# Performance work log

Measured on AMD Instinct MI355X. Metric: run time of the kernel, lower is better.

Reference implementation:

```python
import jax, jax.numpy as jnp
import numpy as np

B, S, D, H = 4, 2048, 1024, 16
HD = D // H

def setup_inputs() -> dict:
    key = jax.random.key(0)
    ks = jax.random.split(key, 5)
    x = jax.random.normal(ks[0], (B, S, D), dtype=jnp.float32)
    mask = jnp.ones((B, S), dtype=jnp.int32)
    # torch nn.Linear init scale ~ 1/sqrt(fan_in); use small normal for stability
    qkv_w = jax.random.normal(ks[1], (3 * D, D), dtype=jnp.float32) * (1.0 / np.sqrt(D))
    qkv_b = jax.random.normal(ks[2], (3 * D,), dtype=jnp.float32) * 0.02
    out_w = jax.random.normal(ks[3], (D, D), dtype=jnp.float32) * (1.0 / np.sqrt(D))
    out_b = jax.random.normal(ks[4], (D,), dtype=jnp.float32) * 0.02
    return {"x": x, "mask": mask, "qkv_w": qkv_w, "qkv_b": qkv_b,
            "out_w": out_w, "out_b": out_b}

def reference(x, mask, qkv_w, qkv_b, out_w, out_b):
    b, s, d = x.shape
    scale = np.sqrt(HD).astype(np.float32)
    # qkv projection: torch Linear y = x @ W^T + b
    qkv = x @ qkv_w.T + qkv_b                      # (b, s, 3d)
    qkv = qkv.reshape(b, s, 3, H, HD)
    qkv = jnp.transpose(qkv, (2, 0, 3, 1, 4))      # (3, b, H, s, hd)
    q, k, v = qkv[0], qkv[1], qkv[2]
    scores = jnp.einsum('bhqd,bhkd->bhqk', q, k) / scale  # (b, H, s, s)
    neg_inf = jnp.float32(-jnp.inf)
    causal = jnp.tril(jnp.ones((s, s), dtype=bool))
    scores = jnp.where(causal[None, None], scores, neg_inf)
    key_mask = (mask != 0)[:, None, None, :]       # (b, 1, 1, s)
    scores = jnp.where(key_mask, scores, neg_inf)
    attn = jax.nn.softmax(scores, axis=-1)
    out = jnp.einsum('bhqk,bhkd->bhqd', attn, v)   # (b, H, s, hd)
    out = jnp.transpose(out, (0, 2, 1, 3)).reshape(b, s, d)
    return out @ out_w.T + out_b
```

## Files before the change

### kernel.cpp

```cpp
#include <hip/hip_runtime.h>
#include <stdint.h>
#include <type_traits>

#define BB  4
#define SS  2048
#define DD  1024
#define HH  16
#define HDD 64

typedef __attribute__((ext_vector_type(8)))  short s16x8;
typedef __attribute__((ext_vector_type(4)))  float f32x4;
typedef __attribute__((ext_vector_type(16))) float f32x16;

__device__ inline short f2bf(float f) {
    union { float f; unsigned int u; } v; v.f = f;
    unsigned int r = (v.u + 0x7fffu + ((v.u >> 16) & 1u)) >> 16;
    return (short)r;
}
__device__ inline unsigned int pack2bf(float a, float b) {
    return (unsigned int)(unsigned short)f2bf(a) | ((unsigned int)(unsigned short)f2bf(b) << 16);
}

#define GLL(gp, lp) __builtin_amdgcn_global_load_lds( \
    (const __attribute__((address_space(1))) void*)(gp), \
    (__attribute__((address_space(3))) void*)(lp), 16, 0, 0)

__global__ void cvt_kernel(const float* __restrict__ src, short* __restrict__ dst, int n) {
    int i = (blockIdx.x * 256 + threadIdx.x) * 8;
    if (i >= n) return;
    const float4* s = (const float4*)(src + i);
    float4 a = s[0], b = s[1];
    s16x8 o;
    o[0]=f2bf(a.x); o[1]=f2bf(a.y); o[2]=f2bf(a.z); o[3]=f2bf(a.w);
    o[4]=f2bf(b.x); o[5]=f2bf(b.y); o[6]=f2bf(b.z); o[7]=f2bf(b.w);
    *(s16x8*)(dst + i) = o;
}

template<int EPI>
__global__ __launch_bounds__(256)
void gemm_bt(const short* __restrict__ A, const short* __restrict__ Bw,
             const float* __restrict__ bias, float* __restrict__ Cf,
             short* __restrict__ Qo, short* __restrict__ Ko, short* __restrict__ Vo,
             int M, int N, int K)
{
    __shared__ short lsA[128 * 32];
    __shared__ short lsB[128 * 32];
    const int tid  = threadIdx.x;
    const int w    = tid >> 6, lane = tid & 63;
    const int quad = lane >> 4, l15 = lane & 15;
    const int m0 = blockIdx.x * 128, n0 = blockIdx.y * 128;
    const int mw = (w & 1) * 64, nw = (w >> 1) * 64;

    f32x4 acc[4][4] = {};

    const int srow = w * 32 + (lane >> 2);
    const int scol = (lane & 3) * 8;
    const short* pA = A + (size_t)(m0 + srow) * K + scol;
    const short* pB = Bw + (size_t)(n0 + srow) * K + scol;
    short* lAbase0 = &lsA[(w * 32) * 32];
    short* lAbase1 = &lsA[(w * 32 + 16) * 32];
    short* lBbase0 = &lsB[(w * 32) * 32];
    short* lBbase1 = &lsB[(w * 32 + 16) * 32];

    for (int kk = 0; kk < K; kk += 32) {
        __syncthreads();
        GLL(pA + kk,            lAbase0);
        GLL(pA + kk + 16 * K,   lAbase1);
        GLL(pB + kk,            lBbase0);
        GLL(pB + kk + 16 * K,   lBbase1);
        asm volatile("s_waitcnt vmcnt(0)" ::: "memory");
        __syncthreads();

        s16x8 af[4], bfr[4];
        for (int t = 0; t < 4; ++t) {
            af[t]  = *(const s16x8*)&lsA[(mw + t * 16 + l15) * 32 + quad * 8];
            bfr[t] = *(const s16x8*)&lsB[(nw + t * 16 + l15) * 32 + quad * 8];
        }
        for (int i = 0; i < 4; ++i)
            for (int j = 0; j < 4; ++j)
                acc[i][j] = __builtin_amdgcn_mfma_f32_16x16x32_bf16(af[i], bfr[j], acc[i][j], 0, 0, 0);
    }

    if (EPI == 0) {
        for (int i = 0; i < 4; ++i) {
            int row = m0 + mw + i * 16 + quad * 4;
            for (int j = 0; j < 4; ++j) {
                int col = n0 + nw + j * 16 + l15;
                float bv = bias[col];
                for (int r = 0; r < 4; ++r)
                    Cf[(size_t)(row + r) * N + col] = acc[i][j][r] + bv;
            }
        }
    } else {
        for (int i = 0; i < 4; ++i) {
            int row = m0 + mw + i * 16 + quad * 4;
            for (int j = 0; j < 4; ++j) {
                int col = n0 + nw + j * 16 + l15;
                float bv = bias[col];
                int sel = col >> 10, h = (col >> 6) & 15, hd = col & 63;
                for (int r = 0; r < 4; ++r) {
                    int rr = row + r;
                    int b = rr >> 11, s = rr & 2047;
                    short val = f2bf(acc[i][j][r] + bv);
                    if (sel == 0)      Qo[(((size_t)b * HH + h) * SS + s) * HDD + hd] = val;
                    else if (sel == 1) Ko[(((size_t)b * HH + h) * SS + s) * HDD + hd] = val;
                    else               Vo[(((size_t)b * HH + h) * HDD + hd) * SS + s] = val;
                }
            }
        }
    }
}

__global__ __launch_bounds__(256, 4)
void attn_kernel(const short* __restrict__ Q, const short* __restrict__ Kb,
                 const short* __restrict__ Vb, const int* __restrict__ mask,
                 short* __restrict__ O)
{
    __shared__ short lsK[128 * 64];
    __shared__ short lsV[64 * 128];
    __shared__ float lsM[128];

    const int tid = threadIdx.x;
    const int w   = tid >> 6, lane = tid & 63;
    const int h   = lane >> 5, q = lane & 31;
    const int bx = blockIdx.x, bh = blockIdx.y;
    const int b = bh >> 4;
    const size_t baseQK = (size_t)bh * SS * HDD;
    const size_t baseV  = (size_t)bh * HDD * SS;
    const float SC = 0.18033688f;

    for (int t = 0; t < 2; ++t) {
        const int qb = t ? bx : (15 - bx);
        const int q0 = qb * 128;
        const int s_row = q0 + w * 32 + q;
        const int T = qb + 1;

        s16x8 bq[4];
        for (int kb = 0; kb < 4; ++kb)
            bq[kb] = *(const s16x8*)(Q + baseQK + (size_t)s_row * HDD + kb * 16 + h * 8);

        float lsum = 0.f;
        f32x16 oa[2] = {};

        auto tile = [&](auto CC, int kt) {
            constexpr bool CAUS = decltype(CC)::value;
            const int kv0 = kt * 128;
            __syncthreads();
            for (int i = 0; i < 4; ++i) {
                const int p0 = w * 256 + i * 64;
                const int p  = p0 + lane;
                const int key = p >> 3, cck = (p & 7) ^ (key & 7);
                GLL(Kb + baseQK + (size_t)(kv0 + key) * HDD + cck * 8, &lsK[p0 * 8]);
                const int hd = p >> 4, ccv = (p & 15) ^ (hd & 15);
                GLL(Vb + baseV + (size_t)hd * SS + kv0 + ccv * 8, &lsV[p0 * 8]);
            }
            if (tid < 32) {
                int4 mv = *(const int4*)(mask + b * SS + kv0 + tid * 4);
                float4 f;
                f.x = mv.x ? 0.f : -1e30f; f.y = mv.y ? 0.f : -1e30f;
                f.z = mv.z ? 0.f : -1e30f; f.w = mv.w ? 0.f : -1e30f;
                *(float4*)&lsM[tid * 4] = f;
            }
            __syncthreads();

            for (int nt = 0; nt < 4; ++nt) {
                f32x16 sa = {};
                for (int kb = 0; kb < 4; ++kb) {
                    const int key = nt * 32 + q;
                    const int cc  = (kb * 2 + h) ^ (key & 7);
                    s16x8 ak = *(const s16x8*)&lsK[(key * 8 + cc) * 8];
                    sa = __builtin_amdgcn_mfma_f32_32x32x16_bf16(ak, bq[kb], sa, 0, 0, 0);
                }
                unsigned int pk2[4][2];
                for (int g = 0; g < 4; ++g) {
                    float4 mq = *(const float4*)&lsM[nt * 32 + 8 * g + 4 * h];
                    float pv[4];
                    for (int r = 0; r < 4; ++r) {
                        float v = sa[g * 4 + r] * SC + ((const float*)&mq)[r];
                        if (CAUS) {
                            int key_l = nt * 32 + r + 8 * g + 4 * h;
                            if (key_l > w * 32 + q) v = -1e30f;
                        }
                        float p = __builtin_amdgcn_exp2f(v);
                        pv[r] = p;
                        lsum += p;
                    }
                    pk2[g][0] = pack2bf(pv[0], pv[1]);
                    pk2[g][1] = pack2bf(pv[2], pv[3]);
                }
                for (int kb2 = 0; kb2 < 2; ++kb2) {
                    const int g_own = 2 * kb2 + h;
                    unsigned int s0 = h ? pk2[2 * kb2][0] : pk2[2 * kb2 + 1][0];
                    unsigned int s1 = h ? pk2[2 * kb2][1] : pk2[2 * kb2 + 1][1];
                    unsigned int r0 = (unsigned int)__shfl_xor((int)s0, 32);
                    unsigned int r1 = (unsigned int)__shfl_xor((int)s1, 32);
                    union { s16x8 v; unsigned int d[4]; } bp;
                    if (h == 0) { bp.d[0] = pk2[g_own][0]; bp.d[1] = pk2[g_own][1]; bp.d[2] = r0; bp.d[3] = r1; }
                    else        { bp.d[0] = r0; bp.d[1] = r1; bp.d[2] = pk2[g_own][0]; bp.d[3] = pk2[g_own][1]; }
                    for (int mt = 0; mt < 2; ++mt) {
                        const int hd = mt * 32 + q;
                        const int cc = ((nt * 2 + kb2) * 2 + h) ^ (hd & 15);
                        s16x8 av = *(const s16x8*)&lsV[(hd * 16 + cc) * 8];
                        oa[mt] = __builtin_amdgcn_mfma_f32_32x32x16_bf16(av, bp.v, oa[mt], 0, 0, 0);
                    }
                }
            }
        };

        for (int kt = 0; kt < T - 1; ++kt) tile(std::false_type{}, kt);
        tile(std::true_type{}, T - 1);

        float ls2 = lsum + __shfl_xor(lsum, 32);
        float inv = 1.0f / ls2;
        const int hcol = (bh & 15) * HDD;
        const size_t obase = ((size_t)b * SS + s_row) * DD + hcol;
        for (int mt = 0; mt < 2; ++mt) {
            for (int g = 0; g < 4; ++g) {
                const int hd0 = mt * 32 + 8 * g + 4 * h;
                unsigned int lo = pack2bf(oa[mt][g * 4 + 0] * inv, oa[mt][g * 4 + 1] * inv);
                unsigned int hi = pack2bf(oa[mt][g * 4 + 2] * inv, oa[mt][g * 4 + 3] * inv);
                uint2 st; st.x = lo; st.y = hi;
                *(uint2*)&O[obase + hd0] = st;
            }
        }
    }
}

extern "C" void kernel_launch(void* const* d_in, const int* in_sizes, int n_in,
                              void* d_out, int out_size, void* d_ws, size_t ws_size,
                              hipStream_t stream) {
    const float* x     = (const float*)d_in[0];
    const int*   mask  = (const int*)d_in[1];
    const float* qkv_w = (const float*)d_in[2];
    const float* qkv_b = (const float*)d_in[3];
    const float* out_w = (const float*)d_in[4];
    const float* out_b = (const float*)d_in[5];
    float* out = (float*)d_out;

    const size_t M1 = (size_t)BB * SS;
    short* ws  = (short*)d_ws;
    short* xb  = ws;
    short* qwb = xb  + M1 * DD;
    short* owb = qwb + (size_t)3 * DD * DD;
    short* Qb  = owb + (size_t)DD * DD;
    short* Kb  = Qb  + M1 * DD;
    short* Vb  = Kb  + M1 * DD;
    short* Ob  = Vb  + M1 * DD;

    cvt_kernel<<<(int)(M1 * DD / 8 / 256), 256, 0, stream>>>(x, xb, (int)(M1 * DD));
    cvt_kernel<<<3 * DD * DD / 8 / 256, 256, 0, stream>>>(qkv_w, qwb, 3 * DD * DD);
    cvt_kernel<<<DD * DD / 8 / 256, 256, 0, stream>>>(out_w, owb, DD * DD);

    gemm_bt<1><<<dim3(64, 24), 256, 0, stream>>>(xb, qwb, qkv_b, nullptr,
                                                 Qb, Kb, Vb, 8192, 3072, 1024);
    attn_kernel<<<dim3(8, BB * HH), 256, 0, stream>>>(Qb, Kb, Vb, mask, Ob);
    gemm_bt<0><<<dim3(64, 8), 256, 0, stream>>>(Ob, owb, out_b, out,
                                                nullptr, nullptr, nullptr, 8192, 1024, 1024);
}
```

Measured before the change: 325.0 us.

## Double-buffer K/V tiles in attention, fold Q scale into projection, one q-block per CTA

The attention kernel now uses 64-key tiles double-buffered in LDS, prefetching the next K/V/mask tile with async global-to-LDS loads while computing the current one, so each tile needs one barrier instead of two. The grid doubles so each block handles a single query block instead of a balanced pair. The softmax scale is folded into Q during the QKV projection epilogue, and bf16 packing uses a byte-permute with simple rounding instead of round-to-nearest-even. Trade-offs are less work balancing per block, a different bf16 rounding mode, and more barriers per unit of work.

```diff
diff --git a/kernel.cpp b/kernel.cpp
--- a/kernel.cpp
+++ b/kernel.cpp
@@ -17,8 +17,9 @@
     unsigned int r = (v.u + 0x7fffu + ((v.u >> 16) & 1u)) >> 16;
     return (short)r;
 }
-__device__ inline unsigned int pack2bf(float a, float b) {
-    return (unsigned int)(unsigned short)f2bf(a) | ((unsigned int)(unsigned short)f2bf(b) << 16);
+__device__ inline unsigned int permpack(float a, float b) {
+    union { float f; unsigned int u; } x, y; x.f = a; y.f = b;
+    return __builtin_amdgcn_perm(y.u + 0x8000u, x.u + 0x8000u, 0x07060302u);
 }
 
 #define GLL(gp, lp) __builtin_amdgcn_global_load_lds( \
@@ -92,6 +93,7 @@
             }
         }
     } else {
+        const float QSC = 0.18033688f;
         for (int i = 0; i < 4; ++i) {
             int row = m0 + mw + i * 16 + quad * 4;
             for (int j = 0; j < 4; ++j) {
@@ -101,10 +103,10 @@
                 for (int r = 0; r < 4; ++r) {
                     int rr = row + r;
                     int b = rr >> 11, s = rr & 2047;
-                    short val = f2bf(acc[i][j][r] + bv);
-                    if (sel == 0)      Qo[(((size_t)b * HH + h) * SS + s) * HDD + hd] = val;
-                    else if (sel == 1) Ko[(((size_t)b * HH + h) * SS + s) * HDD + hd] = val;
-                    else               Vo[(((size_t)b * HH + h) * HDD + hd) * SS + s] = val;
+                    float av = acc[i][j][r] + bv;
+                    if (sel == 0)      Qo[(((size_t)b * HH + h) * SS + s) * HDD + hd] = f2bf(av * QSC);
+                    else if (sel == 1) Ko[(((size_t)b * HH + h) * SS + s) * HDD + hd] = f2bf(av);
+                    else               Vo[(((size_t)b * HH + h) * HDD + hd) * SS + s] = f2bf(av);
                 }
             }
         }
@@ -116,112 +118,137 @@
                  const short* __restrict__ Vb, const int* __restrict__ mask,
                  short* __restrict__ O)
 {
-    __shared__ short lsK[128 * 64];
-    __shared__ short lsV[64 * 128];
-    __shared__ float lsM[128];
+    __shared__ short lsK[2][64 * 64];
+    __shared__ short lsV[2][64 * 64];
+    __shared__ float lsM[2][64];
 
     const int tid = threadIdx.x;
     const int w   = tid >> 6, lane = tid & 63;
     const int h   = lane >> 5, q = lane & 31;
     const int bx = blockIdx.x, bh = blockIdx.y;
+    const int qb = (bx & 1) ? (15 - (bx >> 1)) : (bx >> 1);
     const int b = bh >> 4;
     const size_t baseQK = (size_t)bh * SS * HDD;
     const size_t baseV  = (size_t)bh * HDD * SS;
-    const float SC = 0.18033688f;
-
-    for (int t = 0; t < 2; ++t) {
-        const int qb = t ? bx : (15 - bx);
-        const int q0 = qb * 128;
-        const int s_row = q0 + w * 32 + q;
-        const int T = qb + 1;
-
-        s16x8 bq[4];
-        for (int kb = 0; kb < 4; ++kb)
-            bq[kb] = *(const s16x8*)(Q + baseQK + (size_t)s_row * HDD + kb * 16 + h * 8);
-
-        float lsum = 0.f;
-        f32x16 oa[2] = {};
-
-        auto tile = [&](auto CC, int kt) {
-            constexpr bool CAUS = decltype(CC)::value;
-            const int kv0 = kt * 128;
-            __syncthreads();
-            for (int i = 0; i < 4; ++i) {
-                const int p0 = w * 256 + i * 64;
-                const int p  = p0 + lane;
-                const int key = p >> 3, cck = (p & 7) ^ (key & 7);
-                GLL(Kb + baseQK + (size_t)(kv0 + key) * HDD + cck * 8, &lsK[p0 * 8]);
-                const int hd = p >> 4, ccv = (p & 15) ^ (hd & 15);
-                GLL(Vb + baseV + (size_t)hd * SS + kv0 + ccv * 8, &lsV[p0 * 8]);
-            }
-            if (tid < 32) {
-                int4 mv = *(const int4*)(mask + b * SS + kv0 + tid * 4);
-                float4 f;
-                f.x = mv.x ? 0.f : -1e30f; f.y = mv.y ? 0.f : -1e30f;
-                f.z = mv.z ? 0.f : -1e30f; f.w = mv.w ? 0.f : -1e30f;
-                *(float4*)&lsM[tid * 4] = f;
-            }
-            __syncthreads();
-
-            for (int nt = 0; nt < 4; ++nt) {
-                f32x16 sa = {};
-                for (int kb = 0; kb < 4; ++kb) {
-                    const int key = nt * 32 + q;
-                    const int cc  = (kb * 2 + h) ^ (key & 7);
-                    s16x8 ak = *(const s16x8*)&lsK[(key * 8 + cc) * 8];
-                    sa = __builtin_amdgcn_mfma_f32_32x32x16_bf16(ak, bq[kb], sa, 0, 0, 0);
+    const int q0 = qb * 128;
+    const int s_row = q0 + w * 32 + q;
+    const int T = 2 * (qb + 1);
+
+    s16x8 bq[4];
+    for (int kb = 0; kb < 4; ++kb)
+        bq[kb] = *(const s16x8*)(Q + baseQK + (size_t)s_row * HDD + kb * 16 + h * 8);
+
+    const short* gK[2]; const short* gV[2]; int lofs[2];
+    for (int i = 0; i < 2; ++i) {
+        const int p = w * 128 + i * 64 + lane;
+        const int kr = p >> 3, s = p & 7;
+        gK[i] = Kb + baseQK + (size_t)kr * HDD + ((s ^ (kr & 7)) * 8);
+        gV[i] = Vb + baseV + (size_t)kr * SS + ((s ^ (kr & 7)) * 8);
+        lofs[i] = (w * 128 + i * 64) * 8;
+    }
+    const int* mbase = mask + b * SS;
+
+    float lsum = 0.f;
+    f32x16 oa[2] = {};
+
+    for (int i = 0; i < 2; ++i) {
+        GLL(gK[i], &lsK[0][lofs[i]]);
+        GLL(gV[i], &lsV[0][lofs[i]]);
+    }
+    if (tid < 16) {
+        int4 mv = *(const int4*)(mbase + tid * 4);
+        float4 f;
+        f.x = mv.x ? 0.f : -1e30f; f.y = mv.y ? 0.f : -1e30f;
+        f.z = mv.z ? 0.f : -1e30f; f.w = mv.w ? 0.f : -1e30f;
+        *(float4*)&lsM[0][tid * 4] = f;
+    }
+    __syncthreads();
+
+    auto step = [&](int kt, auto CC) {
+        constexpr bool CAUS = decltype(CC)::value;
+        const int cur = kt & 1, nxt = cur ^ 1;
+        const int kv0 = kt * 64;
+
+        int4 mv;
+        const bool pf = (kt + 1 < T);
+        if (pf) {
+            const size_t okK = (size_t)(kv0 + 64) * HDD;
+            const int   okV = kv0 + 64;
+            for (int i = 0; i < 2; ++i) {
+                GLL(gK[i] + okK, &lsK[nxt][lofs[i]]);
+                GLL(gV[i] + okV, &lsV[nxt][lofs[i]]);
+            }
+            if (tid < 16) mv = *(const int4*)(mbase + kv0 + 64 + tid * 4);
+        }
+
+        for (int nt = 0; nt < 2; ++nt) {
+            f32x16 sa = {};
+            const int key = nt * 32 + q;
+            for (int kb = 0; kb < 4; ++kb) {
+                const int cc = (kb * 2 + h) ^ (key & 7);
+                s16x8 ak = *(const s16x8*)&lsK[cur][(key * 8 + cc) * 8];
+                sa = __builtin_amdgcn_mfma_f32_32x32x16_bf16(ak, bq[kb], sa, 0, 0, 0);
+            }
+            unsigned int pk2[4][2];
+            for (int g = 0; g < 4; ++g) {
+                float4 mq = *(const float4*)&lsM[cur][nt * 32 + 8 * g + 4 * h];
+                float pv[4];
+                for (int r = 0; r < 4; ++r) {
+                    float v = sa[g * 4 + r] + ((const float*)&mq)[r];
+                    if (CAUS) {
+                        int keyg = kv0 + nt * 32 + 8 * g + 4 * h + r;
+                        if (keyg > s_row) v = -1e30f;
+                    }
+                    float p = __builtin_amdgcn_exp2f(v);
+                    pv[r] = p;
+                    lsum += p;
                 }
-                unsigned int pk2[4][2];
-                for (int g = 0; g < 4; ++g) {
-                    float4 mq = *(const float4*)&lsM[nt * 32 + 8 * g + 4 * h];
-                    float pv[4];
-                    for (int r = 0; r < 4; ++r) {
-                        float v = sa[g * 4 + r] * SC + ((const float*)&mq)[r];
-                        if (CAUS) {
-                            int key_l = nt * 32 + r + 8 * g + 4 * h;
-                            if (key_l > w * 32 + q) v = -1e30f;
-                        }
-                        float p = __builtin_amdgcn_exp2f(v);
-                        pv[r] = p;
-                        lsum += p;
-                    }
-                    pk2[g][0] = pack2bf(pv[0], pv[1]);
-                    pk2[g][1] = pack2bf(pv[2], pv[3]);
+                pk2[g][0] = permpack(pv[0], pv[1]);
+                pk2[g][1] = permpack(pv[2], pv[3]);
+            }
+            for (int kb2 = 0; kb2 < 2; ++kb2) {
+                const int g_own = 2 * kb2 + h;
+                unsigned int s0 = h ? pk2[2 * kb2][0] : pk2[2 * kb2 + 1][0];
+                unsigned int s1 = h ? pk2[2 * kb2][1] : pk2[2 * kb2 + 1][1];
+                unsigned int r0 = (unsigned int)__shfl_xor((int)s0, 32);
+                unsigned int r1 = (unsigned int)__shfl_xor((int)s1, 32);
+                union { s16x8 v; unsigned int d[4]; } bp;
+                if (h == 0) { bp.d[0] = pk2[g_own][0]; bp.d[1] = pk2[g_own][1]; bp.d[2] = r0; bp.d[3] = r1; }
+                else        { bp.d[0] = r0; bp.d[1] = r1; bp.d[2] = pk2[g_own][0]; bp.d[3] = pk2[g_own][1]; }
+                for (int mt = 0; mt < 2; ++mt) {
+                    const int hd = mt * 32 + q;
+                    const int cc = (nt * 4 + kb2 * 2 + h) ^ (hd & 7);
+                    s16x8 av = *(const s16x8*)&lsV[cur][(hd * 8 + cc) * 8];
+                    oa[mt] = __builtin_amdgcn_mfma_f32_32x32x16_bf16(av, bp.v, oa[mt], 0, 0, 0);
                 }
-                for (int kb2 = 0; kb2 < 2; ++kb2) {
-                    const int g_own = 2 * kb2 + h;
-                    unsigned int s0 = h ? pk2[2 * kb2][0] : pk2[2 * kb2 + 1][0];
-                    unsigned int s1 = h ? pk2[2 * kb2][1] : pk2[2 * kb2 + 1][1];
-                    unsigned int r0 = (unsigned int)__shfl_xor((int)s0, 32);
-                    unsigned int r1 = (unsigned int)__shfl_xor((int)s1, 32);
-                    union { s16x8 v; unsigned int d[4]; } bp;
-                    if (h == 0) { bp.d[0] = pk2[g_own][0]; bp.d[1] = pk2[g_own][1]; bp.d[2] = r0; bp.d[3] = r1; }
-                    else        { bp.d[0] = r0; bp.d[1] = r1; bp.d[2] = pk2[g_own][0]; bp.d[3] = pk2[g_own][1]; }
-                    for (int mt = 0; mt < 2; ++mt) {
-                        const int hd = mt * 32 + q;
-                        const int cc = ((nt * 2 + kb2) * 2 + h) ^ (hd & 15);
-                        s16x8 av = *(const s16x8*)&lsV[(hd * 16 + cc) * 8];
-                        oa[mt] = __builtin_amdgcn_mfma_f32_32x32x16_bf16(av, bp.v, oa[mt], 0, 0, 0);
-                    }
-                }
-            }
-        };
-
-        for (int kt = 0; kt < T - 1; ++kt) tile(std::false_type{}, kt);
-        tile(std::true_type{}, T - 1);
-
-        float ls2 = lsum + __shfl_xor(lsum, 32);
-        float inv = 1.0f / ls2;
-        const int hcol = (bh & 15) * HDD;
-        const size_t obase = ((size_t)b * SS + s_row) * DD + hcol;
-        for (int mt = 0; mt < 2; ++mt) {
-            for (int g = 0; g < 4; ++g) {
-                const int hd0 = mt * 32 + 8 * g + 4 * h;
-                unsigned int lo = pack2bf(oa[mt][g * 4 + 0] * inv, oa[mt][g * 4 + 1] * inv);
-                unsigned int hi = pack2bf(oa[mt][g * 4 + 2] * inv, oa[mt][g * 4 + 3] * inv);
-                uint2 st; st.x = lo; st.y = hi;
-                *(uint2*)&O[obase + hd0] = st;
-            }
+            }
+        }
+
+        if (pf && tid < 16) {
+            float4 f;
+            f.x = mv.x ? 0.f : -1e30f; f.y = mv.y ? 0.f : -1e30f;
+            f.z = mv.z ? 0.f : -1e30f; f.w = mv.w ? 0.f : -1e30f;
+            *(float4*)&lsM[nxt][tid * 4] = f;
+        }
+        __syncthreads();
+    };
+
+    int kt = 0;
+    for (; kt < T - 2; ++kt) step(kt, std::false_type{});
+    step(kt, std::true_type{}); ++kt;
+    step(kt, std::true_type{});
+
+    float ls2 = lsum + __shfl_xor(lsum, 32);
+    float inv = 1.0f / ls2;
+    const int hcol = (bh & 15) * HDD;
+    const size_t obase = ((size_t)b * SS + s_row) * DD + hcol;
+    for (int mt = 0; mt < 2; ++mt) {
+        for (int g = 0; g < 4; ++g) {
+            const int hd0 = mt * 32 + 8 * g + 4 * h;
+            uint2 st;
+            st.x = permpack(oa[mt][g * 4 + 0] * inv, oa[mt][g * 4 + 1] * inv);
+            st.y = permpack(oa[mt][g * 4 + 2] * inv, oa[mt][g * 4 + 3] * inv);
+            *(uint2*)&O[obase + hd0] = st;
         }
     }
 }
@@ -253,7 +280,7 @@
 
     gemm_bt<1><<<dim3(64, 24), 256, 0, stream>>>(xb, qwb, qkv_b, nullptr,
                                                  Qb, Kb, Vb, 8192, 3072, 1024);
-    attn_kernel<<<dim3(8, BB * HH), 256, 0, stream>>>(Qb, Kb, Vb, mask, Ob);
+    attn_kernel<<<dim3(16, BB * HH), 256, 0, stream>>>(Qb, Kb, Vb, mask, Ob);
     gemm_bt<0><<<dim3(64, 8), 256, 0, stream>>>(Ob, owb, out_b, out,
                                                 nullptr, nullptr, nullptr, 8192, 1024, 1024);
 }
```

Result: slower. 1.266 ms (+289.5%).
